# Performance work log

Measured on AMD Instinct MI355X. Metric: run time of the kernel, lower is better.

Reference implementation:

```python
import jax, jax.numpy as jnp
import numpy as np

N_EMBD = 2048
N_HEAD = 16
HEAD_DIM = 128


def setup_inputs() -> dict:
    key = jax.random.key(0)
    ks = jax.random.split(key, 9)
    B, S = 2, 2048
    s_in = 1.0 / np.sqrt(N_EMBD)
    s_out = 1.0 / np.sqrt(N_HEAD * HEAD_DIM)
    return {
        "x": jax.random.normal(ks[0], (B, S, N_EMBD), dtype=jnp.float32),
        "Wq": jax.random.uniform(ks[1], (N_HEAD * HEAD_DIM, N_EMBD), jnp.float32, -s_in, s_in),
        "bq": jax.random.uniform(ks[2], (N_HEAD * HEAD_DIM,), jnp.float32, -s_in, s_in),
        "Wk": jax.random.uniform(ks[3], (HEAD_DIM, N_EMBD), jnp.float32, -s_in, s_in),
        "bk": jax.random.uniform(ks[4], (HEAD_DIM,), jnp.float32, -s_in, s_in),
        "Wv": jax.random.uniform(ks[5], (HEAD_DIM, N_EMBD), jnp.float32, -s_in, s_in),
        "bv": jax.random.uniform(ks[6], (HEAD_DIM,), jnp.float32, -s_in, s_in),
        "Wo": jax.random.uniform(ks[7], (N_EMBD, N_HEAD * HEAD_DIM), jnp.float32, -s_out, s_out),
        "bo": jax.random.uniform(ks[8], (N_EMBD,), jnp.float32, -s_out, s_out),
    }


def reference(x, Wq, bq, Wk, bk, Wv, bv, Wo, bo):
    B, S, E = x.shape
    H, D = N_HEAD, HEAD_DIM
    q = (x @ Wq.T + bq).reshape(B, S, H, D)        # [B,S,H,D]
    k = x @ Wk.T + bk                              # [B,S,D] shared across heads
    v = x @ Wv.T + bv                              # [B,S,D]
    scale = 1.0 / jnp.sqrt(jnp.asarray(D, x.dtype))
    # QK^T with shared K (no per-head expansion materialized)
    attn = jnp.einsum('bqhd,bkd->bhqk', q * scale, k)  # [B,H,S,S]
    # causal mask: positions j>i set to -inf (masked_fill where mask==0)
    causal = jnp.tril(jnp.ones((S, S), dtype=bool))
    attn = jnp.where(causal[None, None], attn, -jnp.inf)
    attn = jax.nn.softmax(attn, axis=-1)
    out = jnp.einsum('bhqk,bkd->bqhd', attn, v).reshape(B, S, H * D)
    return out @ Wo.T + bo
```

## Files before the change

### kernel.cpp

```cpp
#include <hip/hip_runtime.h>
#include <stdint.h>

typedef __attribute__((ext_vector_type(8))) short bf16x8;
typedef __attribute__((ext_vector_type(4))) float f32x4;
typedef __attribute__((ext_vector_type(4))) unsigned short u16x4;
typedef unsigned short u16;

__device__ __forceinline__ u16 f2bf(float f) {
  union { float f; unsigned u; } x; x.f = f;
  unsigned r = x.u + 0x7fffu + ((x.u >> 16) & 1u);
  return (u16)(r >> 16);
}

__device__ __forceinline__ void load16_lds(const void* g, void* l) {
  __builtin_amdgcn_global_load_lds((const __attribute__((address_space(1))) void*)g,
                                   (__attribute__((address_space(3))) void*)l, 16, 0, 0);
}

__global__ void cvt_all(const float* __restrict__ x, const float* __restrict__ wq,
                        const float* __restrict__ wk, const float* __restrict__ wv,
                        const float* __restrict__ wo,
                        u16* __restrict__ xb, u16* __restrict__ wqb,
                        u16* __restrict__ wkb, u16* __restrict__ wvb,
                        u16* __restrict__ wob) {
  int i = blockIdx.x * 256 + threadIdx.x;
  const float* src; u16* dst; int off;
  if (i < 2097152)      { src = x;  dst = xb;  off = 0; }
  else if (i < 3145728) { src = wq; dst = wqb; off = 2097152; }
  else if (i < 3211264) { src = wk; dst = wkb; off = 3145728; }
  else if (i < 3276800) { src = wv; dst = wvb; off = 3211264; }
  else                  { src = wo; dst = wob; off = 3276800; }
  int j = i - off;
  f32x4 f = ((const f32x4*)src)[j];
  u16x4 o;
  o.x = f2bf(f.x); o.y = f2bf(f.y); o.z = f2bf(f.z); o.w = f2bf(f.w);
  ((u16x4*)dst)[j] = o;
}

__global__ void gemm_qkv(const u16* __restrict__ X, const u16* __restrict__ Wq,
                         const u16* __restrict__ Wk, const u16* __restrict__ Wv,
                         const float* __restrict__ bq, const float* __restrict__ bk,
                         const float* __restrict__ bv, u16* __restrict__ Y,
                         u16* __restrict__ Vt) {
  constexpr int K = 2048, LDY = 2176;
  __shared__ __align__(16) u16 At[128 * 64];
  __shared__ __align__(16) u16 Bt[128 * 64];
  const int bm = blockIdx.x & 31;
  const int bn = blockIdx.x >> 5;
  const int m0 = bm * 128;
  const u16* Wsrc; int nbase;
  if (bn < 16)      { Wsrc = Wq; nbase = bn * 128; }
  else if (bn == 16){ Wsrc = Wk; nbase = 0; }
  else              { Wsrc = Wv; nbase = 0; }
  const int tid = threadIdx.x, wid = tid >> 6, lane = tid & 63;
  const int quad = lane >> 4, l16 = lane & 15;
  const int wm = wid >> 1, wn = wid & 1;
  f32x4 acc[4][4] = {};
  for (int k0 = 0; k0 < K; k0 += 64) {
    __syncthreads();
#pragma unroll
    for (int t = 0; t < 4; t++) {
      int c = t * 256 + tid;
      int row = c >> 3, skc = c & 7, kc = skc ^ (row & 7);
      load16_lds(X + (size_t)(m0 + row) * K + k0 + kc * 8, At + (size_t)(t * 256 + wid * 64) * 8);
      load16_lds(Wsrc + (size_t)(nbase + row) * K + k0 + kc * 8, Bt + (size_t)(t * 256 + wid * 64) * 8);
    }
    asm volatile("s_waitcnt vmcnt(0)" ::: "memory");
    __syncthreads();
#pragma unroll
    for (int ks = 0; ks < 2; ks++) {
      bf16x8 af[4], bfv[4];
#pragma unroll
      for (int mi = 0; mi < 4; mi++) {
        int row = wm * 64 + mi * 16 + l16;
        af[mi] = *(const bf16x8*)(At + (row * 8 + ((ks * 4 + quad) ^ (l16 & 7))) * 8);
      }
#pragma unroll
      for (int ni = 0; ni < 4; ni++) {
        int row = wn * 64 + ni * 16 + l16;
        bfv[ni] = *(const bf16x8*)(Bt + (row * 8 + ((ks * 4 + quad) ^ (l16 & 7))) * 8);
      }
#pragma unroll
      for (int mi = 0; mi < 4; mi++)
#pragma unroll
        for (int ni = 0; ni < 4; ni++)
          acc[mi][ni] = __builtin_amdgcn_mfma_f32_16x16x32_bf16(af[mi], bfv[ni], acc[mi][ni], 0, 0, 0);
    }
  }
  if (bn == 17) {
    int bb = m0 >> 11;
#pragma unroll
    for (int ni = 0; ni < 4; ni++) {
      int d = wn * 64 + ni * 16 + l16;
      float bias = bv[d];
#pragma unroll
      for (int mi = 0; mi < 4; mi++) {
        int m = m0 + wm * 64 + mi * 16 + quad * 4;
        u16x4 pk;
        pk.x = f2bf(acc[mi][ni][0] + bias);
        pk.y = f2bf(acc[mi][ni][1] + bias);
        pk.z = f2bf(acc[mi][ni][2] + bias);
        pk.w = f2bf(acc[mi][ni][3] + bias);
        *(u16x4*)(Vt + (size_t)(bb * 128 + d) * 2048 + (m & 2047)) = pk;
      }
    }
  } else {
    const float* bs = (bn < 16) ? bq : bk;
    const int cbase = (bn < 16) ? bn * 128 : 2048;
    const int bbase = (bn < 16) ? bn * 128 : 0;
#pragma unroll
    for (int ni = 0; ni < 4; ni++) {
      int nl = wn * 64 + ni * 16 + l16;
      float bias = bs[bbase + nl];
#pragma unroll
      for (int mi = 0; mi < 4; mi++) {
        int m = m0 + wm * 64 + mi * 16 + quad * 4;
#pragma unroll
        for (int r = 0; r < 4; r++)
          Y[(size_t)(m + r) * LDY + cbase + nl] = f2bf(acc[mi][ni][r] + bias);
      }
    }
  }
}

__global__ __launch_bounds__(128, 2) void flash_mqa(const u16* __restrict__ Y,
                                                    const u16* __restrict__ Vt,
                                                    u16* __restrict__ Op,
                                                    float* __restrict__ lp) {
  constexpr int LDY = 2176, S = 2048, D = 128;
  __shared__ __align__(16) u16 Kt[64 * 128];
  __shared__ __align__(16) u16 Vts[128 * 64];
  __shared__ __align__(16) u16 Pl[2][32 * 64];
  const int bid = blockIdx.x;
  const int qt = 31 - (bid >> 6);
  const int rem = bid & 63, bh = rem >> 1, half = rem & 1;
  const int b = bh >> 4, h = bh & 15;
  const int q0 = qt * 64;
  const int ntiles = qt + 1, h1 = (ntiles + 1) >> 1;
  const int kt0 = half ? h1 : 0, kt1 = half ? ntiles : h1;
  const int tid = threadIdx.x, wid = tid >> 6, lane = tid & 63;
  const int quad = lane >> 4, l16 = lane & 15;
  const float c1 = 0.08838834764831845f * 1.4426950408889634f;
  const float c2 = 8.0f * 1.4426950408889634f;
  bf16x8 qf[2][4];
#pragma unroll
  for (int a = 0; a < 2; a++) {
    const u16* qrow = Y + (size_t)(b * S + q0 + wid * 32 + a * 16 + l16) * LDY + h * D;
#pragma unroll
    for (int kd = 0; kd < 4; kd++) qf[a][kd] = *(const bf16x8*)(qrow + kd * 32 + quad * 8);
  }
  f32x4 oacc[2][8] = {};
  float ls[2][4] = {};
  for (int kt = kt0; kt < kt1; kt++) {
    const int k0 = kt * 64;
    const bool diag = (kt == qt);
    __syncthreads();
#pragma unroll
    for (int t = 0; t < 8; t++) {
      int c = t * 128 + tid;
      int j = c >> 4, dc = (c & 15) ^ (j & 15);
      load16_lds(Y + (size_t)(b * S + k0 + j) * LDY + 2048 + dc * 8,
                 Kt + (size_t)(t * 128 + wid * 64) * 8);
    }
#pragma unroll
    for (int t = 0; t < 8; t++) {
      int c = t * 128 + tid;
      int d = c >> 3, jc = (c & 7) ^ (d & 7);
      load16_lds(Vt + (size_t)(b * D + d) * S + k0 + jc * 8,
                 Vts + (size_t)(t * 128 + wid * 64) * 8);
    }
    asm volatile("s_waitcnt vmcnt(0)" ::: "memory");
    __syncthreads();
    f32x4 sc[2][4] = {};
#pragma unroll
    for (int kd = 0; kd < 4; kd++) {
      int dch = kd * 4 + quad;
#pragma unroll
      for (int jf = 0; jf < 4; jf++) {
        bf16x8 bb = *(const bf16x8*)(Kt + ((size_t)(jf * 16 + l16) * 16 + (dch ^ l16)) * 8);
        sc[0][jf] = __builtin_amdgcn_mfma_f32_16x16x32_bf16(qf[0][kd], bb, sc[0][jf], 0, 0, 0);
        sc[1][jf] = __builtin_amdgcn_mfma_f32_16x16x32_bf16(qf[1][kd], bb, sc[1][jf], 0, 0, 0);
      }
    }
#pragma unroll
    for (int a = 0; a < 2; a++) {
#pragma unroll
      for (int r = 0; r < 4; r++) {
        float v[4];
#pragma unroll
        for (int jf = 0; jf < 4; jf++) v[jf] = sc[a][jf][r];
        if (diag) {
          int i = q0 + wid * 32 + a * 16 + quad * 4 + r;
#pragma unroll
          for (int jf = 0; jf < 4; jf++)
            if (k0 + jf * 16 + l16 > i) v[jf] = -1e30f;
        }
        float p[4];
#pragma unroll
        for (int jf = 0; jf < 4; jf++) p[jf] = __builtin_amdgcn_exp2f(v[jf] * c1 - c2);
        ls[a][r] += (p[0] + p[1]) + (p[2] + p[3]);
        int m = a * 16 + quad * 4 + r;
#pragma unroll
        for (int jf = 0; jf < 4; jf++) {
          int jc = jf * 2 + (l16 >> 3);
          Pl[wid][((size_t)m * 8 + (jc ^ (m & 7))) * 8 + (l16 & 7)] = f2bf(p[jf]);
        }
      }
    }
    asm volatile("s_waitcnt lgkmcnt(0)" ::: "memory");
#pragma unroll
    for (int cch = 0; cch < 2; cch++) {
      int jcr = cch * 4 + quad;
      bf16x8 pa0 = *(const bf16x8*)(&Pl[wid][((size_t)l16 * 8 + (jcr ^ (l16 & 7))) * 8]);
      bf16x8 pa1 = *(const bf16x8*)(&Pl[wid][((size_t)(16 + l16) * 8 + (jcr ^ (l16 & 7))) * 8]);
#pragma unroll
      for (int nd = 0; nd < 8; nd++) {
        int d = nd * 16 + l16;
        bf16x8 vb = *(const bf16x8*)(Vts + ((size_t)d * 8 + (jcr ^ (d & 7))) * 8);
        oacc[0][nd] = __builtin_amdgcn_mfma_f32_16x16x32_bf16(pa0, vb, oacc[0][nd], 0, 0, 0);
        oacc[1][nd] = __builtin_amdgcn_mfma_f32_16x16x32_bf16(pa1, vb, oacc[1][nd], 0, 0, 0);
      }
    }
  }
  u16* Oph = Op + (size_t)half * 8388608;
  float* lph = lp + (size_t)half * 65536;
#pragma unroll
  for (int a = 0; a < 2; a++) {
#pragma unroll
    for (int r = 0; r < 4; r++) {
      float s = ls[a][r];
#pragma unroll
      for (int off = 1; off < 16; off <<= 1) s += __shfl_xor(s, off, 64);
      int tok = q0 + wid * 32 + a * 16 + quad * 4 + r;
      u16* orow = Oph + (size_t)(b * S + tok) * 2048 + h * D;
#pragma unroll
      for (int nd = 0; nd < 8; nd++)
        orow[nd * 16 + l16] = f2bf(oacc[a][nd][r]);
      if (l16 == 0) lph[(size_t)(b * S + tok) * 16 + h] = s;
    }
  }
}

__global__ void combine(const u16* __restrict__ Op, const float* __restrict__ lp,
                        u16* __restrict__ Ob) {
  int i = blockIdx.x * 256 + threadIdx.x;
  size_t e = (size_t)i * 8;
  int row = i >> 8;
  int h = (i & 255) >> 4;
  float la = lp[(size_t)row * 16 + h], lb = lp[65536 + (size_t)row * 16 + h];
  float inv = 1.0f / (la + lb);
  uint4 pa = *(const uint4*)(Op + e);
  uint4 pb = *(const uint4*)(Op + 8388608 + e);
  const unsigned* ua = (const unsigned*)&pa;
  const unsigned* ub = (const unsigned*)&pb;
  u16 outv[8];
#pragma unroll
  for (int k = 0; k < 4; k++) {
    union { unsigned u; float f; } a0, a1, b0, b1;
    a0.u = (ua[k] & 0xffffu) << 16;  a1.u = ua[k] & 0xffff0000u;
    b0.u = (ub[k] & 0xffffu) << 16;  b1.u = ub[k] & 0xffff0000u;
    outv[k * 2]     = f2bf((a0.f + b0.f) * inv);
    outv[k * 2 + 1] = f2bf((a1.f + b1.f) * inv);
  }
  *(uint4*)(Ob + e) = *(uint4*)outv;
}

__global__ void gemm_out(const u16* __restrict__ A, const u16* __restrict__ W,
                         const float* __restrict__ bias, float* __restrict__ Cout) {
  constexpr int K = 2048, N = 2048;
  __shared__ __align__(16) u16 At[128 * 64];
  __shared__ __align__(16) u16 Bt[128 * 64];
  const int bm = blockIdx.x & 31;
  const int bn = blockIdx.x >> 5;
  const int m0 = bm * 128, n0 = bn * 128;
  const int tid = threadIdx.x, wid = tid >> 6, lane = tid & 63;
  const int quad = lane >> 4, l16 = lane & 15;
  const int wm = wid >> 1, wn = wid & 1;
  f32x4 acc[4][4] = {};
  for (int k0 = 0; k0 < K; k0 += 64) {
    __syncthreads();
#pragma unroll
    for (int t = 0; t < 4; t++) {
      int c = t * 256 + tid;
      int row = c >> 3, kc = (c & 7) ^ (row & 7);
      load16_lds(A + (size_t)(m0 + row) * K + k0 + kc * 8, At + (size_t)(t * 256 + wid * 64) * 8);
      load16_lds(W + (size_t)(n0 + row) * K + k0 + kc * 8, Bt + (size_t)(t * 256 + wid * 64) * 8);
    }
    asm volatile("s_waitcnt vmcnt(0)" ::: "memory");
    __syncthreads();
#pragma unroll
    for (int ks = 0; ks < 2; ks++) {
      bf16x8 af[4], bfv[4];
#pragma unroll
      for (int mi = 0; mi < 4; mi++) {
        int row = wm * 64 + mi * 16 + l16;
        af[mi] = *(const bf16x8*)(At + (row * 8 + ((ks * 4 + quad) ^ (l16 & 7))) * 8);
      }
#pragma unroll
      for (int ni = 0; ni < 4; ni++) {
        int row = wn * 64 + ni * 16 + l16;
        bfv[ni] = *(const bf16x8*)(Bt + (row * 8 + ((ks * 4 + quad) ^ (l16 & 7))) * 8);
      }
#pragma unroll
      for (int mi = 0; mi < 4; mi++)
#pragma unroll
        for (int ni = 0; ni < 4; ni++)
          acc[mi][ni] = __builtin_amdgcn_mfma_f32_16x16x32_bf16(af[mi], bfv[ni], acc[mi][ni], 0, 0, 0);
    }
  }
#pragma unroll
  for (int ni = 0; ni < 4; ni++) {
    int n = n0 + wn * 64 + ni * 16 + l16;
    float bv = bias[n];
#pragma unroll
    for (int mi = 0; mi < 4; mi++) {
      int m = m0 + wm * 64 + mi * 16 + quad * 4;
#pragma unroll
      for (int r = 0; r < 4; r++)
        Cout[(size_t)(m + r) * N + n] = acc[mi][ni][r] + bv;
    }
  }
}

extern "C" void kernel_launch(void* const* d_in, const int* in_sizes, int n_in,
                              void* d_out, int out_size, void* d_ws, size_t ws_size,
                              hipStream_t stream) {
  (void)in_sizes; (void)n_in; (void)out_size; (void)ws_size;
  const float* x  = (const float*)d_in[0];
  const float* Wq = (const float*)d_in[1];
  const float* bq = (const float*)d_in[2];
  const float* Wk = (const float*)d_in[3];
  const float* bk = (const float*)d_in[4];
  const float* Wv = (const float*)d_in[5];
  const float* bv = (const float*)d_in[6];
  const float* Wo = (const float*)d_in[7];
  const float* bo = (const float*)d_in[8];
  float* out = (float*)d_out;

  char* ws = (char*)d_ws;
  size_t off = 0;
  auto carve = [&](size_t bytes) -> char* {
    char* p = ws + off; off += (bytes + 255) & ~(size_t)255; return p;
  };
  u16* xb  = (u16*)carve((size_t)4096 * 2048 * 2);
  u16* wqb = (u16*)carve((size_t)2048 * 2048 * 2);
  u16* wkb = (u16*)carve((size_t)128 * 2048 * 2);
  u16* wvb = (u16*)carve((size_t)128 * 2048 * 2);
  u16* wob = (u16*)carve((size_t)2048 * 2048 * 2);
  u16* Yb  = (u16*)carve((size_t)4096 * 2176 * 2);
  u16* Vtb = (u16*)carve((size_t)2 * 128 * 2048 * 2);
  u16* Ob  = (u16*)carve((size_t)4096 * 2048 * 2);
  u16* Opart = (u16*)carve((size_t)2 * 4096 * 2048 * 2);
  float* lpart = (float*)carve((size_t)2 * 4096 * 16 * 4);

  cvt_all<<<16896, 256, 0, stream>>>(x, Wq, Wk, Wv, Wo, xb, wqb, wkb, wvb, wob);
  gemm_qkv<<<576, 256, 0, stream>>>(xb, wqb, wkb, wvb, bq, bk, bv, Yb, Vtb);
  flash_mqa<<<2048, 128, 0, stream>>>(Yb, Vtb, Opart, lpart);
  combine<<<4096, 256, 0, stream>>>(Opart, lpart, Ob);
  gemm_out<<<512, 256, 0, stream>>>(Ob, wob, bo, out);
}
```

Before: 268.0 us.

## Retile QKV GEMM uniformly and transpose score layout for packed P stores

The QKV projection now treats Wq, Wk and Wv as one contiguous weight matrix with 96-wide N tiles, giving a uniform 768-block grid instead of branching on 18 tile columns. In flash attention the QK^T MFMA operands are swapped, so each lane holds consecutive key positions. This lets P be packed into bf16 pairs and written with 8-byte LDS stores, and it replaces the per-row 4-step shuffle reduction with two shuffles plus a broadcast. The GEMM change depends on the workspace carve placing the three bf16 weight buffers back to back, and the narrower tiles lower per-block reuse.

```diff
diff --git a/kernel.cpp b/kernel.cpp
--- a/kernel.cpp
+++ b/kernel.cpp
@@ -1,4 +1,5 @@
 #include <hip/hip_runtime.h>
+#include <hip/hip_bf16.h>
 #include <stdint.h>
 
 typedef __attribute__((ext_vector_type(8))) short bf16x8;
@@ -10,6 +11,12 @@
   union { float f; unsigned u; } x; x.f = f;
   unsigned r = x.u + 0x7fffu + ((x.u >> 16) & 1u);
   return (u16)(r >> 16);
+}
+
+__device__ __forceinline__ unsigned pkbf(float a, float b) {
+  union { __hip_bfloat162 h; unsigned u; } c;
+  c.h = __float22bfloat162_rn(float2{a, b});
+  return c.u;
 }
 
 __device__ __forceinline__ void load16_lds(const void* g, void* l) {
@@ -37,87 +44,82 @@
   ((u16x4*)dst)[j] = o;
 }
 
-__global__ void gemm_qkv(const u16* __restrict__ X, const u16* __restrict__ Wq,
-                         const u16* __restrict__ Wk, const u16* __restrict__ Wv,
+__global__ void gemm_qkv(const u16* __restrict__ X, const u16* __restrict__ W,
                          const float* __restrict__ bq, const float* __restrict__ bk,
                          const float* __restrict__ bv, u16* __restrict__ Y,
                          u16* __restrict__ Vt) {
   constexpr int K = 2048, LDY = 2176;
   __shared__ __align__(16) u16 At[128 * 64];
-  __shared__ __align__(16) u16 Bt[128 * 64];
+  __shared__ __align__(16) u16 Bt[96 * 64];
   const int bm = blockIdx.x & 31;
   const int bn = blockIdx.x >> 5;
-  const int m0 = bm * 128;
-  const u16* Wsrc; int nbase;
-  if (bn < 16)      { Wsrc = Wq; nbase = bn * 128; }
-  else if (bn == 16){ Wsrc = Wk; nbase = 0; }
-  else              { Wsrc = Wv; nbase = 0; }
+  const int m0 = bm * 128, n0 = bn * 96;
   const int tid = threadIdx.x, wid = tid >> 6, lane = tid & 63;
   const int quad = lane >> 4, l16 = lane & 15;
   const int wm = wid >> 1, wn = wid & 1;
-  f32x4 acc[4][4] = {};
+  f32x4 acc[4][3] = {};
   for (int k0 = 0; k0 < K; k0 += 64) {
     __syncthreads();
 #pragma unroll
     for (int t = 0; t < 4; t++) {
       int c = t * 256 + tid;
-      int row = c >> 3, skc = c & 7, kc = skc ^ (row & 7);
-      load16_lds(X + (size_t)(m0 + row) * K + k0 + kc * 8, At + (size_t)(t * 256 + wid * 64) * 8);
-      load16_lds(Wsrc + (size_t)(nbase + row) * K + k0 + kc * 8, Bt + (size_t)(t * 256 + wid * 64) * 8);
+      int row = c >> 3, kc = (c & 7) ^ (row & 7);
+      load16_lds(X + (size_t)(m0 + row) * K + k0 + kc * 8,
+                 At + (size_t)(t * 256 + wid * 64) * 8);
+    }
+#pragma unroll
+    for (int t = 0; t < 3; t++) {
+      int c = t * 256 + tid;
+      int row = c >> 3, kc = (c & 7) ^ (row & 7);
+      load16_lds(W + (size_t)(n0 + row) * K + k0 + kc * 8,
+                 Bt + (size_t)(t * 256 + wid * 64) * 8);
     }
     asm volatile("s_waitcnt vmcnt(0)" ::: "memory");
     __syncthreads();
 #pragma unroll
     for (int ks = 0; ks < 2; ks++) {
-      bf16x8 af[4], bfv[4];
+      bf16x8 af[4], bfv[3];
 #pragma unroll
       for (int mi = 0; mi < 4; mi++) {
         int row = wm * 64 + mi * 16 + l16;
         af[mi] = *(const bf16x8*)(At + (row * 8 + ((ks * 4 + quad) ^ (l16 & 7))) * 8);
       }
 #pragma unroll
-      for (int ni = 0; ni < 4; ni++) {
-        int row = wn * 64 + ni * 16 + l16;
+      for (int ni = 0; ni < 3; ni++) {
+        int row = wn * 48 + ni * 16 + l16;
         bfv[ni] = *(const bf16x8*)(Bt + (row * 8 + ((ks * 4 + quad) ^ (l16 & 7))) * 8);
       }
 #pragma unroll
       for (int mi = 0; mi < 4; mi++)
 #pragma unroll
-        for (int ni = 0; ni < 4; ni++)
+        for (int ni = 0; ni < 3; ni++)
           acc[mi][ni] = __builtin_amdgcn_mfma_f32_16x16x32_bf16(af[mi], bfv[ni], acc[mi][ni], 0, 0, 0);
     }
   }
-  if (bn == 17) {
-    int bb = m0 >> 11;
-#pragma unroll
-    for (int ni = 0; ni < 4; ni++) {
-      int d = wn * 64 + ni * 16 + l16;
+  const int bb = m0 >> 11;
+#pragma unroll
+  for (int ni = 0; ni < 3; ni++) {
+    int ngrp = n0 + wn * 48 + ni * 16;
+    int n = ngrp + l16;
+    if (ngrp >= 2176) {
+      int d = n - 2176;
       float bias = bv[d];
 #pragma unroll
       for (int mi = 0; mi < 4; mi++) {
         int m = m0 + wm * 64 + mi * 16 + quad * 4;
-        u16x4 pk;
-        pk.x = f2bf(acc[mi][ni][0] + bias);
-        pk.y = f2bf(acc[mi][ni][1] + bias);
-        pk.z = f2bf(acc[mi][ni][2] + bias);
-        pk.w = f2bf(acc[mi][ni][3] + bias);
-        *(u16x4*)(Vt + (size_t)(bb * 128 + d) * 2048 + (m & 2047)) = pk;
-      }
-    }
-  } else {
-    const float* bs = (bn < 16) ? bq : bk;
-    const int cbase = (bn < 16) ? bn * 128 : 2048;
-    const int bbase = (bn < 16) ? bn * 128 : 0;
-#pragma unroll
-    for (int ni = 0; ni < 4; ni++) {
-      int nl = wn * 64 + ni * 16 + l16;
-      float bias = bs[bbase + nl];
+        uint2 pk;
+        pk.x = pkbf(acc[mi][ni][0] + bias, acc[mi][ni][1] + bias);
+        pk.y = pkbf(acc[mi][ni][2] + bias, acc[mi][ni][3] + bias);
+        *(uint2*)(Vt + (size_t)(bb * 128 + d) * 2048 + (m & 2047)) = pk;
+      }
+    } else {
+      float bias = (ngrp < 2048) ? bq[n] : bk[n - 2048];
 #pragma unroll
       for (int mi = 0; mi < 4; mi++) {
         int m = m0 + wm * 64 + mi * 16 + quad * 4;
 #pragma unroll
         for (int r = 0; r < 4; r++)
-          Y[(size_t)(m + r) * LDY + cbase + nl] = f2bf(acc[mi][ni][r] + bias);
+          Y[(size_t)(m + r) * LDY + n] = f2bf(acc[mi][ni][r] + bias);
       }
     }
   }
@@ -130,7 +132,7 @@
   constexpr int LDY = 2176, S = 2048, D = 128;
   __shared__ __align__(16) u16 Kt[64 * 128];
   __shared__ __align__(16) u16 Vts[128 * 64];
-  __shared__ __align__(16) u16 Pl[2][32 * 64];
+  __shared__ __align__(16) u16 Pl[2][2048];
   const int bid = blockIdx.x;
   const int qt = 31 - (bid >> 6);
   const int rem = bid & 63, bh = rem >> 1, half = rem & 1;
@@ -150,7 +152,7 @@
     for (int kd = 0; kd < 4; kd++) qf[a][kd] = *(const bf16x8*)(qrow + kd * 32 + quad * 8);
   }
   f32x4 oacc[2][8] = {};
-  float ls[2][4] = {};
+  float ls[2] = {};
   for (int kt = kt0; kt < kt1; kt++) {
     const int k0 = kt * 64;
     const bool diag = (kt == qt);
@@ -177,42 +179,42 @@
       int dch = kd * 4 + quad;
 #pragma unroll
       for (int jf = 0; jf < 4; jf++) {
-        bf16x8 bb = *(const bf16x8*)(Kt + ((size_t)(jf * 16 + l16) * 16 + (dch ^ l16)) * 8);
-        sc[0][jf] = __builtin_amdgcn_mfma_f32_16x16x32_bf16(qf[0][kd], bb, sc[0][jf], 0, 0, 0);
-        sc[1][jf] = __builtin_amdgcn_mfma_f32_16x16x32_bf16(qf[1][kd], bb, sc[1][jf], 0, 0, 0);
+        bf16x8 kf = *(const bf16x8*)(Kt + ((size_t)(jf * 16 + l16) * 16 + (dch ^ l16)) * 8);
+        sc[0][jf] = __builtin_amdgcn_mfma_f32_16x16x32_bf16(kf, qf[0][kd], sc[0][jf], 0, 0, 0);
+        sc[1][jf] = __builtin_amdgcn_mfma_f32_16x16x32_bf16(kf, qf[1][kd], sc[1][jf], 0, 0, 0);
       }
     }
 #pragma unroll
     for (int a = 0; a < 2; a++) {
-#pragma unroll
-      for (int r = 0; r < 4; r++) {
+      int iq = q0 + wid * 32 + a * 16 + l16;
+#pragma unroll
+      for (int jf = 0; jf < 4; jf++) {
         float v[4];
 #pragma unroll
-        for (int jf = 0; jf < 4; jf++) v[jf] = sc[a][jf][r];
+        for (int r = 0; r < 4; r++) v[r] = sc[a][jf][r];
         if (diag) {
-          int i = q0 + wid * 32 + a * 16 + quad * 4 + r;
-#pragma unroll
-          for (int jf = 0; jf < 4; jf++)
-            if (k0 + jf * 16 + l16 > i) v[jf] = -1e30f;
+          int jbase = k0 + jf * 16 + quad * 4;
+#pragma unroll
+          for (int r = 0; r < 4; r++)
+            if (jbase + r > iq) v[r] = -1e30f;
         }
         float p[4];
 #pragma unroll
-        for (int jf = 0; jf < 4; jf++) p[jf] = __builtin_amdgcn_exp2f(v[jf] * c1 - c2);
-        ls[a][r] += (p[0] + p[1]) + (p[2] + p[3]);
-        int m = a * 16 + quad * 4 + r;
-#pragma unroll
-        for (int jf = 0; jf < 4; jf++) {
-          int jc = jf * 2 + (l16 >> 3);
-          Pl[wid][((size_t)m * 8 + (jc ^ (m & 7))) * 8 + (l16 & 7)] = f2bf(p[jf]);
-        }
+        for (int r = 0; r < 4; r++) p[r] = __builtin_amdgcn_exp2f(v[r] * c1 - c2);
+        ls[a] += (p[0] + p[1]) + (p[2] + p[3]);
+        uint2 pk;
+        pk.x = pkbf(p[0], p[1]);
+        pk.y = pkbf(p[2], p[3]);
+        int cp = (jf * 2 + (quad >> 1)) ^ (l16 & 7);
+        *(uint2*)(&Pl[wid][(size_t)(a * 16 + l16) * 64 + cp * 8 + (quad & 1) * 4]) = pk;
       }
     }
     asm volatile("s_waitcnt lgkmcnt(0)" ::: "memory");
 #pragma unroll
     for (int cch = 0; cch < 2; cch++) {
       int jcr = cch * 4 + quad;
-      bf16x8 pa0 = *(const bf16x8*)(&Pl[wid][((size_t)l16 * 8 + (jcr ^ (l16 & 7))) * 8]);
-      bf16x8 pa1 = *(const bf16x8*)(&Pl[wid][((size_t)(16 + l16) * 8 + (jcr ^ (l16 & 7))) * 8]);
+      bf16x8 pa0 = *(const bf16x8*)(&Pl[wid][(size_t)l16 * 64 + ((jcr ^ (l16 & 7)) * 8)]);
+      bf16x8 pa1 = *(const bf16x8*)(&Pl[wid][(size_t)(16 + l16) * 64 + ((jcr ^ (l16 & 7)) * 8)]);
 #pragma unroll
       for (int nd = 0; nd < 8; nd++) {
         int d = nd * 16 + l16;
@@ -226,17 +228,18 @@
   float* lph = lp + (size_t)half * 65536;
 #pragma unroll
   for (int a = 0; a < 2; a++) {
+    float s = ls[a];
+    s += __shfl_xor(s, 16, 64);
+    s += __shfl_xor(s, 32, 64);
 #pragma unroll
     for (int r = 0; r < 4; r++) {
-      float s = ls[a][r];
-#pragma unroll
-      for (int off = 1; off < 16; off <<= 1) s += __shfl_xor(s, off, 64);
       int tok = q0 + wid * 32 + a * 16 + quad * 4 + r;
       u16* orow = Oph + (size_t)(b * S + tok) * 2048 + h * D;
 #pragma unroll
       for (int nd = 0; nd < 8; nd++)
         orow[nd * 16 + l16] = f2bf(oacc[a][nd][r]);
-      if (l16 == 0) lph[(size_t)(b * S + tok) * 16 + h] = s;
+      float svr = __shfl(s, quad * 4 + r, 64);
+      if (l16 == 0) lph[(size_t)(b * S + tok) * 16 + h] = svr;
     }
   }
 }
@@ -354,7 +357,7 @@
   float* lpart = (float*)carve((size_t)2 * 4096 * 16 * 4);
 
   cvt_all<<<16896, 256, 0, stream>>>(x, Wq, Wk, Wv, Wo, xb, wqb, wkb, wvb, wob);
-  gemm_qkv<<<576, 256, 0, stream>>>(xb, wqb, wkb, wvb, bq, bk, bv, Yb, Vtb);
+  gemm_qkv<<<768, 256, 0, stream>>>(xb, wqb, bq, bk, bv, Yb, Vtb);
   flash_mqa<<<2048, 128, 0, stream>>>(Yb, Vtb, Opart, lpart);
   combine<<<4096, 256, 0, stream>>>(Opart, lpart, Ob);
   gemm_out<<<512, 256, 0, stream>>>(Ob, wob, bo, out);
```

After: 263.5 us. No clear change (-1.7%).
